# Kernel tuning notes

Hardware: AMD Instinct MI355X
Metric: run time of the kernel (lower is better)

Reference implementation:

```python
import jax, jax.numpy as jnp
import numpy as np

N = 100000      # num_nodes
E = 1600000     # num edges (avg degree 16)
R = 400         # num_relations passed to GCNLayer (masks at R and 2R)
DIN, DH, DOUT = 128, 128, 128
EPS = 1e-5


def setup_inputs() -> dict:
    key = jax.random.key(0)
    ks = jax.random.split(key, 8)
    src = jax.random.randint(ks[0], (E,), 0, N)
    dst = jax.random.randint(ks[1], (E,), 0, N)
    rel = jax.random.randint(ks[2], (E,), 0, 2 * R + 1)  # covers orig/inverse/self-loop buckets
    edges = jnp.stack([src, rel, dst], axis=1)  # [E,3] = (head, rel, tail)

    def xinit(k, shape, fan_in):
        return jax.random.normal(k, shape, jnp.float32) * (1.0 / np.sqrt(fan_in))

    node_emb = xinit(ks[3], (N, DIN), DIN)
    # stacked relation-branch linears: [3, out, in] = (original, inverse, self_loop)
    W1 = xinit(ks[4], (3, DH, DIN), DIN)
    b1 = jnp.zeros((3, DH), jnp.float32)
    Ws1 = xinit(ks[5], (DH, DIN), DIN)
    bs1 = jnp.zeros((DH,), jnp.float32)
    g1 = jnp.ones((DH,), jnp.float32)
    be1 = jnp.zeros((DH,), jnp.float32)
    W2 = xinit(ks[6], (3, DOUT, DH), DH)
    b2 = jnp.zeros((3, DOUT), jnp.float32)
    Ws2 = xinit(ks[7], (DOUT, DH), DH)
    bs2 = jnp.zeros((DOUT,), jnp.float32)
    g2 = jnp.ones((DOUT,), jnp.float32)
    be2 = jnp.zeros((DOUT,), jnp.float32)
    return dict(edges=edges, node_emb=node_emb, W1=W1, b1=b1, Ws1=Ws1, bs1=bs1,
                g1=g1, be1=be1, W2=W2, b2=b2, Ws2=Ws2, bs2=bs2, g2=g2, be2=be2)


def _gcn_layer(x, src, dst, bucket, W, b):
    # Project node features once per relation branch (same math as projecting
    # gathered src features, but N << E so this is cheaper): Y[r] = x @ W[r].T + b[r]
    Y = jnp.einsum('nd,rod->rno', x, W) + b[:, None, :]     # [3, N, out]
    msgs = Y[bucket, src]                                   # [E, out] gather by (branch, src)
    n = x.shape[0]
    out = jax.ops.segment_sum(msgs, dst, num_segments=n)    # scatter-add to dst
    cnt = jax.ops.segment_sum(jnp.ones_like(dst, dtype=x.dtype), dst, num_segments=n)
    out = out / jnp.maximum(cnt, 1.0)[:, None]              # degree norm, clamp min=1
    return jax.nn.relu(out)


def _layer_norm(x, g, b):
    m = jnp.mean(x, axis=-1, keepdims=True)
    v = jnp.mean((x - m) ** 2, axis=-1, keepdims=True)
    return (x - m) * jax.lax.rsqrt(v + EPS) * g + b


def reference(edges, node_emb, W1, b1, Ws1, bs1, g1, be1, W2, b2, Ws2, bs2, g2, be2):
    src, rel, dst = edges[:, 0], edges[:, 1], edges[:, 2]
    # bucket: 0=original (rel<R), 1=inverse (R<=rel<2R), 2=self-loop (rel>=2R)
    bucket = (rel >= R).astype(jnp.int32) + (rel >= 2 * R).astype(jnp.int32)

    x1 = _gcn_layer(node_emb, src, dst, bucket, W1, b1)
    x1 = x1 + node_emb @ Ws1.T + bs1                # skip1
    x1 = _layer_norm(x1, g1, be1)                   # dropout: eval-mode identity

    x2 = _gcn_layer(x1, src, dst, bucket, W2, b2)
    x2 = x2 + x1 @ Ws2.T + bs2                      # skip2
    x2 = _layer_norm(x2, g2, be2)
    return x2
```

## Files before the change

kernel.cpp:

```cpp
#include <hip/hip_runtime.h>
#include <stdint.h>

typedef unsigned int uint;
typedef unsigned short ushort;

#define NNODES 100000
#define NPAD   100096
#define NEDGES 1600000
#define RCONST 400
#define CAP    64
#define ZROW   NNODES

#define NBKT   196
#define NBLK_A 512
#define EPB    3125
#define RUNCAP 64
#define NCONVX 25024

typedef __attribute__((ext_vector_type(8))) short short8;
typedef __attribute__((ext_vector_type(4))) float f32x4;

__device__ __forceinline__ float bflo(uint u){ union{uint i;float f;}c; c.i=u<<16; return c.f; }
__device__ __forceinline__ float bfhi(uint u){ union{uint i;float f;}c; c.i=u&0xFFFF0000u; return c.f; }
__device__ __forceinline__ ushort f2bf(float f){ union{uint i;float ff;}c; c.ff=f; uint u=c.i;
    return (ushort)((u + 0x7FFFu + ((u>>16)&1u))>>16); }
__device__ __forceinline__ uint pack2(float lo, float hi){
    return (uint)f2bf(lo) | ((uint)f2bf(hi)<<16); }


__global__ __launch_bounds__(256) void binfill_kernel(const int* __restrict__ edges,
                                                      int* __restrict__ runcnt,
                                                      uint* __restrict__ binned) {
    __shared__ int pos[NBKT];
    int blk = blockIdx.x, tid = threadIdx.x;
    for (int i = tid; i < NBKT; i += 256) pos[i] = 0;
    __syncthreads();
    int start = blk * EPB;
    for (int i = tid; i < EPB; i += 256) {
        int e = start + i;
        int src = edges[e * 3];
        int rel = edges[e * 3 + 1];
        int dst = edges[e * 3 + 2];
        int bkt = (rel >= RCONST) + (rel >= 2 * RCONST);
        int b = dst >> 9, off = dst & 511;
        int p = atomicAdd(&pos[b], 1);
        if (p < RUNCAP)
            binned[((size_t)b * NBLK_A + blk) * RUNCAP + p] =
                (uint)src | ((uint)bkt << 17) | ((uint)off << 19);
    }
    __syncthreads();
    for (int i = tid; i < NBKT; i += 256)
        runcnt[blk * NBKT + i] = min(pos[i], RUNCAP);
}


__global__ __launch_bounds__(256) void scatterx_kernel(
    const uint* __restrict__ binned, const int* __restrict__ runcnt,
    int* __restrict__ elist, uint* __restrict__ segp, float4* __restrict__ cnts,
    const float* __restrict__ x, uint* __restrict__ xb,
    const float* __restrict__ W1, const float* __restrict__ Ws1, uint* __restrict__ Wb1,
    const float* __restrict__ W2, const float* __restrict__ Ws2, uint* __restrict__ Wb2) {
    __shared__ int cnt3[512][4];
    __shared__ int cur[512][4];
    int blk = blockIdx.x, tid = threadIdx.x;

    if (blk < NBKT) {
        int b = blk;
        int base = b << 9;
        for (int i = tid; i < 512; i += 256) { cnt3[i][0] = 0; cnt3[i][1] = 0; cnt3[i][2] = 0; }
        __syncthreads();
        #pragma unroll
        for (int rr = 0; rr < 2; ++rr) {
            int r = tid * 2 + rr;
            int n = runcnt[r * NBKT + b];
            const uint* p = binned + ((size_t)b * NBLK_A + r) * RUNCAP;
            for (int i = 0; i < n; ++i) {
                uint e = p[i];
                atomicAdd(&cnt3[e >> 19][(e >> 17) & 3], 1);
            }
        }
        __syncthreads();
        for (int i = tid; i < 512; i += 256) {
            int node = base + i;
            if (node >= NPAD) continue;
            int c0 = cnt3[i][0], c1 = cnt3[i][1], c2 = cnt3[i][2];
            int n0 = min((c0 + 1) & ~1, 64);
            int n1 = min((c1 + 1) & ~1, 64 - n0);
            int n2 = min((c2 + 1) & ~1, 64 - n0 - n1);
            int s1 = n0, s2 = n0 + n1;
            cur[i][0] = 0; cur[i][1] = s1; cur[i][2] = s2;
            int* er = elist + (size_t)node * 64;
            for (int j = min(c0, n0); j < n0; ++j) er[j] = ZROW;
            for (int j = min(c1, n1); j < n1; ++j) er[s1 + j] = ZROW;
            for (int j = min(c2, n2); j < n2; ++j) er[s2 + j] = ZROW;
            cnt3[i][0] = s1; cnt3[i][1] = s2; cnt3[i][2] = s2 + n2;
            segp[node] = (uint)n0 | ((uint)n1 << 8) | ((uint)n2 << 16);
            float4 v;
            v.x = (float)c0; v.y = (float)c1; v.z = (float)c2;
            v.w = 1.0f / fmaxf((float)(c0 + c1 + c2), 1.0f);
            cnts[node] = v;
        }
        __syncthreads();
        #pragma unroll
        for (int rr = 0; rr < 2; ++rr) {
            int r = tid * 2 + rr;
            int n = runcnt[r * NBKT + b];
            const uint* p = binned + ((size_t)b * NBLK_A + r) * RUNCAP;
            for (int i = 0; i < n; ++i) {
                uint e = p[i];
                int off = (int)(e >> 19), bk = (int)((e >> 17) & 3);
                int pos = atomicAdd(&cur[off][bk], 1);
                if (pos < cnt3[off][bk])
                    elist[(size_t)(base + off) * 64 + pos] = (int)(e & 0x7FFFFu);
            }
        }
    } else if (blk < NBKT + NCONVX) {
        size_t i = (size_t)(blk - NBKT) * 256 + tid;
        if (i < (size_t)NPAD * 64) {
            uint val = 0;
            if (i < (size_t)NNODES * 64) {
                float2 f = *(const float2*)&x[i * 2];
                val = pack2(f.x, f.y);
            }
            xb[i] = val;
        }
    } else {
        int wi = blk - (NBKT + NCONVX);
        const float* W  = (wi < 128) ? W1  : W2;
        const float* Ws = (wi < 128) ? Ws1 : Ws2;
        uint* Wb        = (wi < 128) ? Wb1 : Wb2;
        int i = (wi & 127) * 256 + tid;
        int n = i >> 8, kp = i & 255, k = kp * 2;
        float v0, v1;
        if (k < 384) {
            int r = k >> 7, kk = k & 127;
            const float* p = W + r * 16384 + n * 128 + kk;
            v0 = p[0]; v1 = p[1];
        } else {
            const float* p = Ws + n * 128 + (k - 384);
            v0 = p[0]; v1 = p[1];
        }
        Wb[i] = pack2(v0, v1);
    }
}


__global__ __launch_bounds__(256) void gather_kernel(
    const uint* __restrict__ xbu,
    const uint* __restrict__ segp,
    const int*  __restrict__ elist,
    const float4* __restrict__ cnts,
    uint* __restrict__ Ab) {
    int w = threadIdx.x >> 6, lane = threadIdx.x & 63;
    int node = blockIdx.x * 4 + w;
    uint sp = __builtin_amdgcn_readfirstlane(segp[node]);
    int tot = (int)(sp & 255) + (int)((sp >> 8) & 255) + (int)((sp >> 16) & 255);
    float inv = cnts[node].w;
    int ve = elist[(size_t)node * 64 + lane];

    float a0l = 0.f, a0h = 0.f, a1l = 0.f, a1h = 0.f, a2l = 0.f, a2h = 0.f;
    int j = 0;
    for (; j + 4 <= tot; j += 4) {
        int e0 = __builtin_amdgcn_readlane(ve, j);
        int e1 = __builtin_amdgcn_readlane(ve, j + 1);
        int e2 = __builtin_amdgcn_readlane(ve, j + 2);
        int e3 = __builtin_amdgcn_readlane(ve, j + 3);
        int s0 = e0 & 0x1FFFF, k0 = e0 >> 17;
        int s1 = e1 & 0x1FFFF, k1 = e1 >> 17;
        int s2 = e2 & 0x1FFFF, k2 = e2 >> 17;
        int s3 = e3 & 0x1FFFF, k3 = e3 >> 17;
        uint u0 = xbu[((size_t)s0 << 6) + lane];
        uint u1 = xbu[((size_t)s1 << 6) + lane];
        uint u2 = xbu[((size_t)s2 << 6) + lane];
        uint u3 = xbu[((size_t)s3 << 6) + lane];

        float q00 = (k0 == 0) ? 1.f : 0.f, q01 = (k0 == 1) ? 1.f : 0.f, q02 = (k0 == 2) ? 1.f : 0.f;
        float q10 = (k1 == 0) ? 1.f : 0.f, q11 = (k1 == 1) ? 1.f : 0.f, q12 = (k1 == 2) ? 1.f : 0.f;
        float q20 = (k2 == 0) ? 1.f : 0.f, q21 = (k2 == 1) ? 1.f : 0.f, q22 = (k2 == 2) ? 1.f : 0.f;
        float q30 = (k3 == 0) ? 1.f : 0.f, q31 = (k3 == 1) ? 1.f : 0.f, q32 = (k3 == 2) ? 1.f : 0.f;

        float f0l = bflo(u0), f0h = bfhi(u0);
        float f1l = bflo(u1), f1h = bfhi(u1);
        float f2l = bflo(u2), f2h = bfhi(u2);
        float f3l = bflo(u3), f3h = bfhi(u3);

        a0l = fmaf(q00, f0l, a0l); a1l = fmaf(q01, f0l, a1l); a2l = fmaf(q02, f0l, a2l);
        a0h = fmaf(q00, f0h, a0h); a1h = fmaf(q01, f0h, a1h); a2h = fmaf(q02, f0h, a2h);
        a0l = fmaf(q10, f1l, a0l); a1l = fmaf(q11, f1l, a1l); a2l = fmaf(q12, f1l, a2l);
        a0h = fmaf(q10, f1h, a0h); a1h = fmaf(q11, f1h, a1h); a2h = fmaf(q12, f1h, a2h);
        a0l = fmaf(q20, f2l, a0l); a1l = fmaf(q21, f2l, a1l); a2l = fmaf(q22, f2l, a2l);
        a0h = fmaf(q20, f2h, a0h); a1h = fmaf(q21, f2h, a1h); a2h = fmaf(q22, f2h, a2h);
        a0l = fmaf(q30, f3l, a0l); a1l = fmaf(q31, f3l, a1l); a2l = fmaf(q32, f3l, a2l);
        a0h = fmaf(q30, f3h, a0h); a1h = fmaf(q31, f3h, a1h); a2h = fmaf(q32, f3h, a2h);
    }
    if (j < tot) {
        int e0 = __builtin_amdgcn_readlane(ve, j);
        int e1 = __builtin_amdgcn_readlane(ve, j + 1);
        int s0 = e0 & 0x1FFFF, k0 = e0 >> 17;
        int s1 = e1 & 0x1FFFF, k1 = e1 >> 17;
        uint u0 = xbu[((size_t)s0 << 6) + lane];
        uint u1 = xbu[((size_t)s1 << 6) + lane];
        float q00 = (k0 == 0) ? 1.f : 0.f, q01 = (k0 == 1) ? 1.f : 0.f, q02 = (k0 == 2) ? 1.f : 0.f;
        float q10 = (k1 == 0) ? 1.f : 0.f, q11 = (k1 == 1) ? 1.f : 0.f, q12 = (k1 == 2) ? 1.f : 0.f;
        float f0l = bflo(u0), f0h = bfhi(u0);
        float f1l = bflo(u1), f1h = bfhi(u1);
        a0l = fmaf(q00, f0l, a0l); a1l = fmaf(q01, f0l, a1l); a2l = fmaf(q02, f0l, a2l);
        a0h = fmaf(q00, f0h, a0h); a1h = fmaf(q01, f0h, a1h); a2h = fmaf(q02, f0h, a2h);
        a0l = fmaf(q10, f1l, a0l); a1l = fmaf(q11, f1l, a1l); a2l = fmaf(q12, f1l, a2l);
        a0h = fmaf(q10, f1h, a0h); a1h = fmaf(q11, f1h, a1h); a2h = fmaf(q12, f1h, a2h);
    }

    size_t ab = (size_t)node * 192 + lane;
    Ab[ab]       = pack2(a0l * inv, a0h * inv);
    Ab[ab + 64]  = pack2(a1l * inv, a1h * inv);
    Ab[ab + 128] = pack2(a2l * inv, a2h * inv);
}


template<bool OUT_BF16>
__global__ __launch_bounds__(512, 2) void gemm_kernel(
    const ushort* __restrict__ Ab,
    const ushort* __restrict__ xb,
    const ushort* __restrict__ Wb,
    const float* __restrict__ bia,
    const float* __restrict__ bs,
    const float* __restrict__ g,
    const float* __restrict__ be,
    const float4* __restrict__ cnts,
    void* __restrict__ out) {
    __shared__ ushort lA[128 * 64];
    __shared__ ushort lB[128 * 64];
    __shared__ float sS1[4][128], sS2[4][128];
    __shared__ float sMean[128], sRstd[128];

    int tid = threadIdx.x;
    int w = tid >> 6, lane = tid & 63;
    int wm = w >> 2, wn = w & 3;
    int quad = lane >> 4, l15 = lane & 15;
    int node0 = blockIdx.x * 128;

    int srow = tid >> 2, sseg = (tid & 3) * 2;
    uint swzS = (uint)((srow & 7) << 4);
    uint swzR = (uint)((l15 & 7) << 4);

    const ushort* gA = Ab + (size_t)node0 * 384;
    const ushort* gX = xb + (size_t)node0 * 128;

    f32x4 accm[4][2], accq[4][2];
    f32x4 zero = {0.f, 0.f, 0.f, 0.f};
    #pragma unroll
    for (int i = 0; i < 4; ++i)
        #pragma unroll
        for (int j = 0; j < 2; ++j) { accm[i][j] = zero; accq[i][j] = zero; }

    uint4 ra0, ra1, rb0, rb1;
    auto load_chunk = [&](int t) {
        const ushort* srcA; size_t strA;
        if (t < 6) { srcA = gA + t * 64;       strA = 384; }
        else       { srcA = gX + (t - 6) * 64; strA = 128; }
        const ushort* pa = srcA + (size_t)srow * strA + sseg * 8;
        ra0 = *(const uint4*)(pa);
        ra1 = *(const uint4*)(pa + 8);
        const ushort* pb = Wb + t * 64 + (size_t)srow * 512 + sseg * 8;
        rb0 = *(const uint4*)(pb);
        rb1 = *(const uint4*)(pb + 8);
    };
    auto compute = [&](f32x4 (&acc)[4][2]) {
        #pragma unroll
        for (int ks = 0; ks < 2; ++ks) {
            short8 aF[4], bF[2];
            #pragma unroll
            for (int mt = 0; mt < 4; ++mt) {
                int row = wm * 64 + mt * 16 + l15;
                aF[mt] = *(const short8*)((const char*)lA + row * 128 +
                                          (((uint)(ks * 64 + quad * 16)) ^ swzR));
            }
            #pragma unroll
            for (int nt = 0; nt < 2; ++nt) {
                int row = wn * 32 + nt * 16 + l15;
                bF[nt] = *(const short8*)((const char*)lB + row * 128 +
                                          (((uint)(ks * 64 + quad * 16)) ^ swzR));
            }
            #pragma unroll
            for (int mt = 0; mt < 4; ++mt)
                #pragma unroll
                for (int nt = 0; nt < 2; ++nt)
                    acc[mt][nt] = __builtin_amdgcn_mfma_f32_16x16x32_bf16(
                        aF[mt], bF[nt], acc[mt][nt], 0, 0, 0);
        }
    };

    load_chunk(0);
    for (int t = 0; t < 8; ++t) {
        if (t) __syncthreads();
        {
            char* bA = (char*)lA + srow * 128;
            *(uint4*)(bA + (((uint)(sseg * 16)) ^ swzS))       = ra0;
            *(uint4*)(bA + (((uint)((sseg + 1) * 16)) ^ swzS)) = ra1;
            char* bB = (char*)lB + srow * 128;
            *(uint4*)(bB + (((uint)(sseg * 16)) ^ swzS))       = rb0;
            *(uint4*)(bB + (((uint)((sseg + 1) * 16)) ^ swzS)) = rb1;
        }
        __syncthreads();
        if (t < 7) load_chunk(t + 1);
        if (t < 6) compute(accm); else compute(accq);
    }

    int nl0 = wn * 32 + l15;
    float pb0[2], pb1[2], pb2[2], pbs[2], pg[2], pbe[2];
    #pragma unroll
    for (int nt = 0; nt < 2; ++nt) {
        int nl = nl0 + nt * 16;
        pb0[nt] = bia[nl]; pb1[nt] = bia[128 + nl]; pb2[nt] = bia[256 + nl];
        pbs[nt] = bs[nl];  pg[nt] = g[nl];          pbe[nt] = be[nl];
    }
    #pragma unroll
    for (int mt = 0; mt < 4; ++mt) {
        #pragma unroll
        for (int r = 0; r < 4; ++r) {
            int ml = wm * 64 + mt * 16 + quad * 4 + r;
            float4 c4 = cnts[node0 + ml];
            float s1 = 0.f, s2 = 0.f;
            #pragma unroll
            for (int nt = 0; nt < 2; ++nt) {
                float bd = (c4.x * pb0[nt] + c4.y * pb1[nt] + c4.z * pb2[nt]) * c4.w;
                float v = fmaxf(accm[mt][nt][r] + bd, 0.f) + accq[mt][nt][r] + pbs[nt];
                accm[mt][nt][r] = v;
                s1 += v; s2 += v * v;
            }
            #pragma unroll
            for (int mask = 1; mask < 16; mask <<= 1) {
                s1 += __shfl_xor(s1, mask);
                s2 += __shfl_xor(s2, mask);
            }
            if (l15 == 0) { sS1[wn][ml] = s1; sS2[wn][ml] = s2; }
        }
    }
    __syncthreads();
    if (tid < 128) {
        float s1 = sS1[0][tid] + sS1[1][tid] + sS1[2][tid] + sS1[3][tid];
        float s2 = sS2[0][tid] + sS2[1][tid] + sS2[2][tid] + sS2[3][tid];
        float mean = s1 * (1.f / 128.f);
        float var = s2 * (1.f / 128.f) - mean * mean;
        sMean[tid] = mean;
        sRstd[tid] = rsqrtf(var + 1e-5f);
    }
    __syncthreads();
    #pragma unroll
    for (int mt = 0; mt < 4; ++mt) {
        #pragma unroll
        for (int r = 0; r < 4; ++r) {
            int ml = wm * 64 + mt * 16 + quad * 4 + r;
            int node = node0 + ml;
            float mn = sMean[ml], rs = sRstd[ml];
            #pragma unroll
            for (int nt = 0; nt < 2; ++nt) {
                float v = (accm[mt][nt][r] - mn) * rs * pg[nt] + pbe[nt];
                if (OUT_BF16) {
                    float vh = __shfl_xor(v, 1);
                    if (!(l15 & 1)) {
                        uint val = (node < NNODES) ? pack2(v, vh) : 0u;
                        uint* o = (uint*)out;
                        o[(size_t)node * 64 + wn * 16 + nt * 8 + (l15 >> 1)] = val;
                    }
                } else {
                    if (node < NNODES) {
                        float* o = (float*)out;
                        o[(size_t)node * 128 + nl0 + nt * 16] = v;
                    }
                }
            }
        }
    }
}


extern "C" void kernel_launch(void* const* d_in, const int* in_sizes, int n_in,
                              void* d_out, int out_size, void* d_ws, size_t ws_size,
                              hipStream_t stream) {
    (void)in_sizes; (void)n_in; (void)out_size; (void)ws_size;

    const int*   edges = (const int*)d_in[0];
    const float* xemb  = (const float*)d_in[1];
    const float* W1  = (const float*)d_in[2];
    const float* b1  = (const float*)d_in[3];
    const float* Ws1 = (const float*)d_in[4];
    const float* bs1 = (const float*)d_in[5];
    const float* g1  = (const float*)d_in[6];
    const float* be1 = (const float*)d_in[7];
    const float* W2  = (const float*)d_in[8];
    const float* b2  = (const float*)d_in[9];
    const float* Ws2 = (const float*)d_in[10];
    const float* bs2 = (const float*)d_in[11];
    const float* g2  = (const float*)d_in[12];
    const float* be2 = (const float*)d_in[13];

    char* ws = (char*)d_ws;
    auto take = [&](size_t bytes) {
        char* p = ws;
        ws += (bytes + 255) & ~(size_t)255;
        return p;
    };
    int*    elist  = (int*)take((size_t)NPAD * CAP * 4);
    uint*   segp   = (uint*)take((size_t)NPAD * 4);
    float4* cnts   = (float4*)take((size_t)NPAD * 16);
    uint*   xb0    = (uint*)take((size_t)NPAD * 128 * 2);
    uint*   xb1    = (uint*)take((size_t)NPAD * 128 * 2);
    uint*   Ab     = (uint*)take((size_t)NPAD * 384 * 2);
    uint*   Wb1    = (uint*)take((size_t)128 * 512 * 2);
    uint*   Wb2    = (uint*)take((size_t)128 * 512 * 2);
    int*    runcnt = (int*)take((size_t)NBLK_A * NBKT * 4);
    uint*   binned = (uint*)take((size_t)NBKT * NBLK_A * RUNCAP * 4);

    binfill_kernel<<<NBLK_A, 256, 0, stream>>>(edges, runcnt, binned);
    scatterx_kernel<<<NBKT + NCONVX + 256, 256, 0, stream>>>(
        binned, runcnt, elist, segp, cnts,
        xemb, xb0, W1, Ws1, Wb1, W2, Ws2, Wb2);

    gather_kernel<<<NNODES / 4, 256, 0, stream>>>(xb0, segp, elist, cnts, Ab);
    gemm_kernel<true><<<NPAD / 128, 512, 0, stream>>>(
        (const ushort*)Ab, (const ushort*)xb0, (const ushort*)Wb1,
        b1, bs1, g1, be1, cnts, xb1);

    gather_kernel<<<NNODES / 4, 256, 0, stream>>>(xb1, segp, elist, cnts, Ab);
    gemm_kernel<false><<<NPAD / 128, 512, 0, stream>>>(
        (const ushort*)Ab, (const ushort*)xb1, (const ushort*)Wb2,
        b2, bs2, g2, be2, cnts, d_out);
}
```

Baseline: 394.6 us.

## Pre-swizzle GEMM operand images and load them into LDS via global_load_lds

The gather kernel now writes aggregated features in a per-tile, pre-swizzled LDS image layout, and the weight prep writes weights in the same swizzled image. The GEMM then streams A and B chunks straight into shared memory with global_load_lds, skipping register staging. The skip-path x operand is preloaded into registers up front. This removes VGPR round trips and swizzle arithmetic in the GEMM main loop. The cost is losing the previous register-prefetch overlap between loads and MFMA, since loads now issue and are waited on within the same iteration.

```diff
diff --git a/kernel.cpp b/kernel.cpp
--- a/kernel.cpp
+++ b/kernel.cpp
@@ -26,6 +26,13 @@
     return (ushort)((u + 0x7FFFu + ((u>>16)&1u))>>16); }
 __device__ __forceinline__ uint pack2(float lo, float hi){
     return (uint)f2bf(lo) | ((uint)f2bf(hi)<<16); }
+
+__device__ __forceinline__ void gll16(const void* g, void* l) {
+    __builtin_amdgcn_global_load_lds(
+        (const __attribute__((address_space(1))) uint32_t*)g,
+        (__attribute__((address_space(3))) uint32_t*)l,
+        16, 0, 0);
+}
 
 
 __global__ __launch_bounds__(256) void binfill_kernel(const int* __restrict__ edges,
@@ -130,15 +137,18 @@
         const float* Ws = (wi < 128) ? Ws1 : Ws2;
         uint* Wb        = (wi < 128) ? Wb1 : Wb2;
         int i = (wi & 127) * 256 + tid;
-        int n = i >> 8, kp = i & 255, k = kp * 2;
+        int r = (i >> 5) & 127;
+        int s = (i >> 2) & 7;
+        int p = i & 3;
+        int o = s ^ (r & 7);
+        int k = (i >> 12) * 64 + o * 8 + p * 2;
         float v0, v1;
         if (k < 384) {
-            int r = k >> 7, kk = k & 127;
-            const float* p = W + r * 16384 + n * 128 + kk;
-            v0 = p[0]; v1 = p[1];
+            const float* q = W + (k >> 7) * 16384 + r * 128 + (k & 127);
+            v0 = q[0]; v1 = q[1];
         } else {
-            const float* p = Ws + n * 128 + (k - 384);
-            v0 = p[0]; v1 = p[1];
+            const float* q = Ws + r * 128 + (k - 384);
+            v0 = q[0]; v1 = q[1];
         }
         Wb[i] = pack2(v0, v1);
     }
@@ -150,7 +160,7 @@
     const uint* __restrict__ segp,
     const int*  __restrict__ elist,
     const float4* __restrict__ cnts,
-    uint* __restrict__ Ab) {
+    uint* __restrict__ AbImg) {
     int w = threadIdx.x >> 6, lane = threadIdx.x & 63;
     int node = blockIdx.x * 4 + w;
     uint sp = __builtin_amdgcn_readfirstlane(segp[node]);
@@ -210,26 +220,33 @@
         a0h = fmaf(q10, f1h, a0h); a1h = fmaf(q11, f1h, a1h); a2h = fmaf(q12, f1h, a2h);
     }
 
-    size_t ab = (size_t)node * 192 + lane;
-    Ab[ab]       = pack2(a0l * inv, a0h * inv);
-    Ab[ab + 64]  = pack2(a1l * inv, a1h * inv);
-    Ab[ab + 128] = pack2(a2l * inv, a2h * inv);
+    int r = node & 127;
+    size_t tb = (size_t)(node >> 7) * 24576;
+    int o = (lane >> 2) & 7;
+    int half = lane >> 5;
+    int li = lane & 3;
+    size_t a0 = tb + (size_t)(0 + half) * 4096 + r * 32 + (o ^ (r & 7)) * 4 + li;
+    size_t a1 = tb + (size_t)(2 + half) * 4096 + r * 32 + (o ^ (r & 7)) * 4 + li;
+    size_t a2 = tb + (size_t)(4 + half) * 4096 + r * 32 + (o ^ (r & 7)) * 4 + li;
+    AbImg[a0] = pack2(a0l * inv, a0h * inv);
+    AbImg[a1] = pack2(a1l * inv, a1h * inv);
+    AbImg[a2] = pack2(a2l * inv, a2h * inv);
 }
 
 
 template<bool OUT_BF16>
 __global__ __launch_bounds__(512, 2) void gemm_kernel(
-    const ushort* __restrict__ Ab,
+    const uint* __restrict__ AbImg,
     const ushort* __restrict__ xb,
-    const ushort* __restrict__ Wb,
+    const uint* __restrict__ WbImg,
     const float* __restrict__ bia,
     const float* __restrict__ bs,
     const float* __restrict__ g,
     const float* __restrict__ be,
     const float4* __restrict__ cnts,
     void* __restrict__ out) {
-    __shared__ ushort lA[128 * 64];
-    __shared__ ushort lB[128 * 64];
+    __shared__ __attribute__((aligned(16))) ushort lA[128 * 64];
+    __shared__ __attribute__((aligned(16))) ushort lB[128 * 64];
     __shared__ float sS1[4][128], sS2[4][128];
     __shared__ float sMean[128], sRstd[128];
 
@@ -243,8 +260,22 @@
     uint swzS = (uint)((srow & 7) << 4);
     uint swzR = (uint)((l15 & 7) << 4);
 
-    const ushort* gA = Ab + (size_t)node0 * 384;
-    const ushort* gX = xb + (size_t)node0 * 128;
+    uint4 rx[2][2];
+    {
+        const ushort* gX = xb + (size_t)node0 * 128;
+        #pragma unroll
+        for (int c = 0; c < 2; ++c) {
+            const ushort* pa = gX + (size_t)srow * 128 + c * 64 + sseg * 8;
+            rx[c][0] = *(const uint4*)(pa);
+            rx[c][1] = *(const uint4*)(pa + 8);
+        }
+    }
+
+    const char* aimg = (const char*)(AbImg + (size_t)blockIdx.x * 24576);
+    const char* bimg = (const char*)WbImg;
+    char* ldsA = (char*)lA + w * 2048;
+    char* ldsB = (char*)lB + w * 2048;
+    int loff = w * 2048 + lane * 16;
 
     f32x4 accm[4][2], accq[4][2];
     f32x4 zero = {0.f, 0.f, 0.f, 0.f};
@@ -253,18 +284,6 @@
         #pragma unroll
         for (int j = 0; j < 2; ++j) { accm[i][j] = zero; accq[i][j] = zero; }
 
-    uint4 ra0, ra1, rb0, rb1;
-    auto load_chunk = [&](int t) {
-        const ushort* srcA; size_t strA;
-        if (t < 6) { srcA = gA + t * 64;       strA = 384; }
-        else       { srcA = gX + (t - 6) * 64; strA = 128; }
-        const ushort* pa = srcA + (size_t)srow * strA + sseg * 8;
-        ra0 = *(const uint4*)(pa);
-        ra1 = *(const uint4*)(pa + 8);
-        const ushort* pb = Wb + t * 64 + (size_t)srow * 512 + sseg * 8;
-        rb0 = *(const uint4*)(pb);
-        rb1 = *(const uint4*)(pb + 8);
-    };
     auto compute = [&](f32x4 (&acc)[4][2]) {
         #pragma unroll
         for (int ks = 0; ks < 2; ++ks) {
@@ -290,19 +309,21 @@
         }
     };
 
-    load_chunk(0);
+    #pragma unroll
     for (int t = 0; t < 8; ++t) {
         if (t) __syncthreads();
-        {
+        if (t < 6) {
+            gll16(aimg + t * 16384 + loff,        ldsA);
+            gll16(aimg + t * 16384 + loff + 1024, ldsA + 1024);
+        } else {
+            int c = t - 6;
             char* bA = (char*)lA + srow * 128;
-            *(uint4*)(bA + (((uint)(sseg * 16)) ^ swzS))       = ra0;
-            *(uint4*)(bA + (((uint)((sseg + 1) * 16)) ^ swzS)) = ra1;
-            char* bB = (char*)lB + srow * 128;
-            *(uint4*)(bB + (((uint)(sseg * 16)) ^ swzS))       = rb0;
-            *(uint4*)(bB + (((uint)((sseg + 1) * 16)) ^ swzS)) = rb1;
-        }
+            *(uint4*)(bA + (((uint)(sseg * 16)) ^ swzS))       = rx[c][0];
+            *(uint4*)(bA + (((uint)((sseg + 1) * 16)) ^ swzS)) = rx[c][1];
+        }
+        gll16(bimg + t * 16384 + loff,        ldsB);
+        gll16(bimg + t * 16384 + loff + 1024, ldsB + 1024);
         __syncthreads();
-        if (t < 7) load_chunk(t + 1);
         if (t < 6) compute(accm); else compute(accq);
     }
 
@@ -406,7 +427,7 @@
     float4* cnts   = (float4*)take((size_t)NPAD * 16);
     uint*   xb0    = (uint*)take((size_t)NPAD * 128 * 2);
     uint*   xb1    = (uint*)take((size_t)NPAD * 128 * 2);
-    uint*   Ab     = (uint*)take((size_t)NPAD * 384 * 2);
+    uint*   AbImg  = (uint*)take((size_t)NPAD * 384 * 2);
     uint*   Wb1    = (uint*)take((size_t)128 * 512 * 2);
     uint*   Wb2    = (uint*)take((size_t)128 * 512 * 2);
     int*    runcnt = (int*)take((size_t)NBLK_A * NBKT * 4);
@@ -417,13 +438,13 @@
         binned, runcnt, elist, segp, cnts,
         xemb, xb0, W1, Ws1, Wb1, W2, Ws2, Wb2);
 
-    gather_kernel<<<NNODES / 4, 256, 0, stream>>>(xb0, segp, elist, cnts, Ab);
+    gather_kernel<<<NNODES / 4, 256, 0, stream>>>(xb0, segp, elist, cnts, AbImg);
     gemm_kernel<true><<<NPAD / 128, 512, 0, stream>>>(
-        (const ushort*)Ab, (const ushort*)xb0, (const ushort*)Wb1,
+        AbImg, (const ushort*)xb0, Wb1,
         b1, bs1, g1, be1, cnts, xb1);
 
-    gather_kernel<<<NNODES / 4, 256, 0, stream>>>(xb1, segp, elist, cnts, Ab);
+    gather_kernel<<<NNODES / 4, 256, 0, stream>>>(xb1, segp, elist, cnts, AbImg);
     gemm_kernel<false><<<NPAD / 128, 512, 0, stream>>>(
-        (const ushort*)Ab, (const ushort*)xb1, (const ushort*)Wb2,
+        AbImg, (const ushort*)xb1, Wb2,
         b2, bs2, g2, be2, cnts, d_out);
 }
```

Result: slower. 410.8 us (+4.1%).

## Double-buffer GEMM LDS tiles and vectorize binned-edge reads in bucket pass

Applied to the files above, without the earlier changes.

The GEMM kernel now keeps two LDS buffers for the A and B tiles and alternates between them, which drops one of the two block barriers per k-chunk; the loop is fully unrolled. The CSR build pass reads the binned edge words four at a time with uint4 loads instead of scalar loads. This doubles the GEMM's LDS footprint, which may reduce occupancy at 2 blocks per CU. The uint4 reads can go past n within the RUNCAP slot, which assumes suitable alignment and padding.

```diff
diff --git a/kernel.cpp b/kernel.cpp
--- a/kernel.cpp
+++ b/kernel.cpp
@@ -74,9 +74,12 @@
             int r = tid * 2 + rr;
             int n = runcnt[r * NBKT + b];
             const uint* p = binned + ((size_t)b * NBLK_A + r) * RUNCAP;
-            for (int i = 0; i < n; ++i) {
-                uint e = p[i];
-                atomicAdd(&cnt3[e >> 19][(e >> 17) & 3], 1);
+            for (int i = 0; i < n; i += 4) {
+                uint4 e4 = *(const uint4*)(p + i);
+                atomicAdd(&cnt3[e4.x >> 19][(e4.x >> 17) & 3], 1);
+                if (i + 1 < n) atomicAdd(&cnt3[e4.y >> 19][(e4.y >> 17) & 3], 1);
+                if (i + 2 < n) atomicAdd(&cnt3[e4.z >> 19][(e4.z >> 17) & 3], 1);
+                if (i + 3 < n) atomicAdd(&cnt3[e4.w >> 19][(e4.w >> 17) & 3], 1);
             }
         }
         __syncthreads();
@@ -106,12 +109,19 @@
             int r = tid * 2 + rr;
             int n = runcnt[r * NBKT + b];
             const uint* p = binned + ((size_t)b * NBLK_A + r) * RUNCAP;
-            for (int i = 0; i < n; ++i) {
-                uint e = p[i];
-                int off = (int)(e >> 19), bk = (int)((e >> 17) & 3);
-                int pos = atomicAdd(&cur[off][bk], 1);
-                if (pos < cnt3[off][bk])
-                    elist[(size_t)(base + off) * 64 + pos] = (int)(e & 0x7FFFFu);
+            for (int i = 0; i < n; i += 4) {
+                uint4 e4 = *(const uint4*)(p + i);
+                uint es[4] = { e4.x, e4.y, e4.z, e4.w };
+                #pragma unroll
+                for (int k = 0; k < 4; ++k) {
+                    if (i + k < n) {
+                        uint e = es[k];
+                        int off = (int)(e >> 19), bk = (int)((e >> 17) & 3);
+                        int pos = atomicAdd(&cur[off][bk], 1);
+                        if (pos < cnt3[off][bk])
+                            elist[(size_t)(base + off) * 64 + pos] = (int)(e & 0x7FFFFu);
+                    }
+                }
             }
         }
     } else if (blk < NBKT + NCONVX) {
@@ -228,8 +238,8 @@
     const float* __restrict__ be,
     const float4* __restrict__ cnts,
     void* __restrict__ out) {
-    __shared__ ushort lA[128 * 64];
-    __shared__ ushort lB[128 * 64];
+    __shared__ ushort lA[2][128 * 64];
+    __shared__ ushort lB[2][128 * 64];
     __shared__ float sS1[4][128], sS2[4][128];
     __shared__ float sMean[128], sRstd[128];
 
@@ -265,20 +275,20 @@
         rb0 = *(const uint4*)(pb);
         rb1 = *(const uint4*)(pb + 8);
     };
-    auto compute = [&](f32x4 (&acc)[4][2]) {
+    auto compute = [&](f32x4 (&acc)[4][2], int cb) {
         #pragma unroll
         for (int ks = 0; ks < 2; ++ks) {
             short8 aF[4], bF[2];
             #pragma unroll
             for (int mt = 0; mt < 4; ++mt) {
                 int row = wm * 64 + mt * 16 + l15;
-                aF[mt] = *(const short8*)((const char*)lA + row * 128 +
+                aF[mt] = *(const short8*)((const char*)lA[cb] + row * 128 +
                                           (((uint)(ks * 64 + quad * 16)) ^ swzR));
             }
             #pragma unroll
             for (int nt = 0; nt < 2; ++nt) {
                 int row = wn * 32 + nt * 16 + l15;
-                bF[nt] = *(const short8*)((const char*)lB + row * 128 +
+                bF[nt] = *(const short8*)((const char*)lB[cb] + row * 128 +
                                           (((uint)(ks * 64 + quad * 16)) ^ swzR));
             }
             #pragma unroll
@@ -291,19 +301,20 @@
     };
 
     load_chunk(0);
+    #pragma unroll
     for (int t = 0; t < 8; ++t) {
-        if (t) __syncthreads();
+        int cb = t & 1;
         {
-            char* bA = (char*)lA + srow * 128;
+            char* bA = (char*)lA[cb] + srow * 128;
             *(uint4*)(bA + (((uint)(sseg * 16)) ^ swzS))       = ra0;
             *(uint4*)(bA + (((uint)((sseg + 1) * 16)) ^ swzS)) = ra1;
-            char* bB = (char*)lB + srow * 128;
+            char* bB = (char*)lB[cb] + srow * 128;
             *(uint4*)(bB + (((uint)(sseg * 16)) ^ swzS))       = rb0;
             *(uint4*)(bB + (((uint)((sseg + 1) * 16)) ^ swzS)) = rb1;
         }
         __syncthreads();
         if (t < 7) load_chunk(t + 1);
-        if (t < 6) compute(accm); else compute(accq);
+        if (t < 6) compute(accm, cb); else compute(accq, cb);
     }
 
     int nl0 = wn * 32 + l15;
```

Result: no change. 389.2 us (-1.4%).
